# Performance work log

Hardware: AMD Instinct MI355X
Metric: run time of the kernel (lower is better)

## Reference

```python
import jax, jax.numpy as jnp
import numpy as np

EPS = 1e-5

def _layernorm(x, gamma, beta):
    mu = jnp.mean(x, axis=-1, keepdims=True)
    var = jnp.var(x, axis=-1, keepdims=True)
    return (x - mu) * jax.lax.rsqrt(var + EPS) * gamma + beta

def setup_inputs() -> dict:
    key = jax.random.key(0)
    ks = jax.random.split(key, 6)
    bs, t, dim = 4, 2048, 1024
    x = jax.random.normal(ks[0], (bs, t, dim), dtype=jnp.float32)
    # shared LayerNorm params (same module applied twice in forward)
    ln_gamma = jnp.ones((dim,), dtype=jnp.float32)
    ln_beta = jnp.zeros((dim,), dtype=jnp.float32)
    # Linear params, stored as (in, out)
    w1 = jax.random.normal(ks[1], (dim, 2 * dim), dtype=jnp.float32) / np.sqrt(dim)
    b1 = jax.random.normal(ks[2], (2 * dim,), dtype=jnp.float32) * 0.01
    w2 = jax.random.normal(ks[3], (2 * dim, dim), dtype=jnp.float32) / np.sqrt(2 * dim)
    b2 = jax.random.normal(ks[4], (dim,), dtype=jnp.float32) * 0.01
    return {"x": x, "ln_gamma": ln_gamma, "ln_beta": ln_beta,
            "w1": w1, "b1": b1, "w2": w2, "b2": b2}

def reference(x, ln_gamma, ln_beta, w1, b1, w2, b2):
    # x: [bs, t, f]
    y = _layernorm(x, ln_gamma, ln_beta)
    y = jax.nn.gelu(jnp.einsum('btf,fh->bth', y, w1) + b1, approximate=False)
    y = jnp.einsum('bth,hf->btf', y, w2) + b2
    # attention-like quadratic mix (no softmax): (x @ x^T) @ y
    scores = jnp.einsum('btf,bsf->bts', x, x)          # [bs, t, t]
    y = jnp.einsum('bts,bsf->btf', scores, y)
    y = x + y
    y = _layernorm(y, ln_gamma, ln_beta)
    return y
```

## Files before the change

kernel.cpp:

```cpp
#include <hip/hip_runtime.h>
#include <hip/hip_fp16.h>

typedef _Float16 f16;
typedef _Float16 f16x8 __attribute__((ext_vector_type(8)));
typedef _Float16 f16x4 __attribute__((ext_vector_type(4)));
typedef float f32x4 __attribute__((ext_vector_type(4)));

#define LN_EPS 1e-5f

__device__ __forceinline__ float erf_fast(float x) {
    const float ax = __builtin_fabsf(x);
    const float t = 1.0f / (1.0f + 0.3275911f * ax);
    const float y = t * (0.254829592f +
                    t * (-0.284496736f +
                    t * (1.421413741f +
                    t * (-1.453152027f +
                    t * 1.061405429f))));
    const float r = 1.0f - y * __expf(-ax * ax);
    return __builtin_copysignf(r, x);
}

__device__ __forceinline__ float gelu_exact(float v) {
    return 0.5f * v * (1.0f + erf_fast(v * 0.70710678118654752440f));
}

__device__ __forceinline__ void gload_lds16(const f16* g, f16* l) {
    __builtin_amdgcn_global_load_lds(
        (const __attribute__((address_space(1))) unsigned int*)(g),
        (__attribute__((address_space(3))) unsigned int*)(l),
        16, 0, 0);
}

__global__ __launch_bounds__(256)
void ln_cast_kernel(const float* __restrict__ x,
                    const float* __restrict__ gamma,
                    const float* __restrict__ beta,
                    f16* __restrict__ y_h,
                    f16* __restrict__ x_h) {
    const int row = blockIdx.x;
    const int t = threadIdx.x;
    const size_t base = (size_t)row * 1024;
    float4 v = ((const float4*)(x + base))[t];
    float s  = v.x + v.y + v.z + v.w;
    float s2 = v.x*v.x + v.y*v.y + v.z*v.z + v.w*v.w;
    #pragma unroll
    for (int off = 32; off > 0; off >>= 1) {
        s  += __shfl_down(s, off, 64);
        s2 += __shfl_down(s2, off, 64);
    }
    __shared__ float ls[4], ls2[4];
    const int wid = t >> 6;
    if ((t & 63) == 0) { ls[wid] = s; ls2[wid] = s2; }
    __syncthreads();
    if (t == 0) {
        ls[0]  = ls[0] + ls[1] + ls[2] + ls[3];
        ls2[0] = ls2[0] + ls2[1] + ls2[2] + ls2[3];
    }
    __syncthreads();
    const float mu   = ls[0] * (1.0f / 1024.0f);
    const float var  = ls2[0] * (1.0f / 1024.0f) - mu * mu;
    const float rstd = rsqrtf(var + LN_EPS);
    const float4 g  = ((const float4*)gamma)[t];
    const float4 bt = ((const float4*)beta)[t];
    f16x4 yo, xo;
    yo[0] = (f16)((v.x - mu) * rstd * g.x + bt.x);
    yo[1] = (f16)((v.y - mu) * rstd * g.y + bt.y);
    yo[2] = (f16)((v.z - mu) * rstd * g.z + bt.z);
    yo[3] = (f16)((v.w - mu) * rstd * g.w + bt.w);
    xo[0] = (f16)v.x; xo[1] = (f16)v.y; xo[2] = (f16)v.z; xo[3] = (f16)v.w;
    *(f16x4*)(y_h + base + t * 4) = yo;
    *(f16x4*)(x_h + base + t * 4) = xo;
}

__global__ __launch_bounds__(256)
void ln_final_kernel(const float* __restrict__ pre,
                     const float* __restrict__ gamma,
                     const float* __restrict__ beta,
                     float* __restrict__ out) {
    const int row = blockIdx.x;
    const int t = threadIdx.x;
    const size_t base = (size_t)row * 1024;
    float4 v = ((const float4*)(pre + base))[t];
    float s  = v.x + v.y + v.z + v.w;
    float s2 = v.x*v.x + v.y*v.y + v.z*v.z + v.w*v.w;
    #pragma unroll
    for (int off = 32; off > 0; off >>= 1) {
        s  += __shfl_down(s, off, 64);
        s2 += __shfl_down(s2, off, 64);
    }
    __shared__ float ls[4], ls2[4];
    const int wid = t >> 6;
    if ((t & 63) == 0) { ls[wid] = s; ls2[wid] = s2; }
    __syncthreads();
    if (t == 0) {
        ls[0]  = ls[0] + ls[1] + ls[2] + ls[3];
        ls2[0] = ls2[0] + ls2[1] + ls2[2] + ls2[3];
    }
    __syncthreads();
    const float mu   = ls[0] * (1.0f / 1024.0f);
    const float var  = ls2[0] * (1.0f / 1024.0f) - mu * mu;
    const float rstd = rsqrtf(var + LN_EPS);
    const float4 g  = ((const float4*)gamma)[t];
    const float4 bt = ((const float4*)beta)[t];
    float4 o;
    o.x = (v.x - mu) * rstd * g.x + bt.x;
    o.y = (v.y - mu) * rstd * g.y + bt.y;
    o.z = (v.z - mu) * rstd * g.z + bt.z;
    o.w = (v.w - mu) * rstd * g.w + bt.w;
    ((float4*)(out + base))[t] = o;
}

__global__ __launch_bounds__(256)
void transpose_cast_kernel(const float* __restrict__ src,
                           f16* __restrict__ dst, int R, int C) {
    __shared__ float tile[32][33];
    const int c0 = blockIdx.x * 32, r0 = blockIdx.y * 32;
    const int tx = threadIdx.x & 31, ty = threadIdx.x >> 5;
    #pragma unroll
    for (int i = 0; i < 4; ++i) {
        const int r = ty + i * 8;
        tile[r][tx] = src[(size_t)(r0 + r) * C + c0 + tx];
    }
    __syncthreads();
    #pragma unroll
    for (int i = 0; i < 4; ++i) {
        const int r = ty + i * 8;
        dst[(size_t)(c0 + r) * R + r0 + tx] = (f16)tile[tx][r];
    }
}

__global__ __launch_bounds__(256)
void transpose_f16_kernel(const f16* __restrict__ src,
                          f16* __restrict__ dst, int R, int C) {
    __shared__ f16 tile[32][33];
    const size_t zb = (size_t)blockIdx.z * R * C;
    src += zb; dst += zb;
    const int c0 = blockIdx.x * 32, r0 = blockIdx.y * 32;
    const int tx = threadIdx.x & 31, ty = threadIdx.x >> 5;
    #pragma unroll
    for (int i = 0; i < 4; ++i) {
        const int r = ty + i * 8;
        tile[r][tx] = src[(size_t)(r0 + r) * C + c0 + tx];
    }
    __syncthreads();
    #pragma unroll
    for (int i = 0; i < 4; ++i) {
        const int r = ty + i * 8;
        dst[(size_t)(c0 + r) * R + r0 + tx] = tile[tx][r];
    }
}

template <int EPI>
__global__ __launch_bounds__(512, 2)
void gemm256_nt_kernel(const f16* __restrict__ A, const f16* __restrict__ Bt,
                       const float* __restrict__ bias, f16* __restrict__ outH,
                       int M, int N, int K) {
    __shared__ __attribute__((aligned(16))) f16 sAbuf[2][256 * 64];
    __shared__ __attribute__((aligned(16))) f16 sBbuf[2][256 * 64];

    const int m0 = blockIdx.x * 256;
    const int n0 = blockIdx.y * 256;
    const int t = threadIdx.x;
    const int l = t & 63;
    const int wid = t >> 6;
    const int wr = wid >> 2;
    const int wc = wid & 3;
    const int rl = l & 15;
    const int g  = l >> 4;
    const int nk = K >> 6;

    const int rowS = wid * 16 + (l >> 3);
    const int kbS  = ((l & 7) ^ ((l >> 3) & 7)) * 8;
    const f16* pA = A  + (size_t)(m0 + rowS) * K + kbS;
    const f16* pB = Bt + (size_t)(n0 + rowS) * K + kbS;
    const int ldsS = wid * 1024;

    const int rA = wr * 128 + rl;
    const int rB = wc * 64 + rl;
    const int swk0 = ((g)     ^ (rl & 7)) * 8;
    const int swk1 = ((4 + g) ^ (rl & 7)) * 8;

    f32x4 acc[8][4] = {};

    const long long hstep = (long long)128 * K;

    auto stgA = [&](f16* dst, int h, int kc) {
        const f16* s = pA + (size_t)h * hstep + kc * 64;
        f16* d = dst + h * 8192 + ldsS;
        gload_lds16(s, d);
        gload_lds16(s + 8 * K, d + 512);
    };
    auto stgB = [&](f16* dst, int h, int kc) {
        const f16* s = pB + (size_t)h * hstep + kc * 64;
        f16* d = dst + h * 8192 + ldsS;
        gload_lds16(s, d);
        gload_lds16(s + 8 * K, d + 512);
    };

    f16* bufA0 = sAbuf[0]; f16* bufA1 = sAbuf[1];
    f16* bufB0 = sBbuf[0]; f16* bufB1 = sBbuf[1];

    const int t1 = (nk > 1) ? 1 : 0;
    stgA(bufA0, 0, 0); stgA(bufA0, 1, 0);
    stgB(bufB0, 0, 0); stgB(bufB0, 1, 0);
    stgB(bufB1, 0, t1); stgB(bufB1, 1, t1);
    stgA(bufA1, 0, t1);
    asm volatile("s_waitcnt vmcnt(6)" ::: "memory");
    __builtin_amdgcn_s_barrier();

    f16 *Ac = bufA0, *Ao = bufA1, *Bc = bufB0, *Bo = bufB1;

    f16x8 a[4][2], b0r[2][2], b1r[2][2];

    for (int kt = 0; kt < nk; ++kt) {
        const int kt1 = (kt + 1 < nk) ? kt + 1 : nk - 1;
        const int kt2 = (kt + 2 < nk) ? kt + 2 : nk - 1;

        #pragma unroll
        for (int fm = 0; fm < 4; ++fm) {
            a[fm][0] = *(const f16x8*)(Ac + (rA + fm * 16) * 64 + swk0);
            a[fm][1] = *(const f16x8*)(Ac + (rA + fm * 16) * 64 + swk1);
        }
        #pragma unroll
        for (int fn = 0; fn < 2; ++fn) {
            b0r[fn][0] = *(const f16x8*)(Bc + (rB + fn * 16) * 64 + swk0);
            b0r[fn][1] = *(const f16x8*)(Bc + (rB + fn * 16) * 64 + swk1);
        }
        stgA(Ao, 1, kt1);
        __builtin_amdgcn_s_barrier();
        asm volatile("s_waitcnt lgkmcnt(0)" ::: "memory");
        __builtin_amdgcn_sched_barrier(0);
        __builtin_amdgcn_s_setprio(1);
        #pragma unroll
        for (int fm = 0; fm < 4; ++fm)
            #pragma unroll
            for (int fn = 0; fn < 2; ++fn) {
                acc[fm][fn] = __builtin_amdgcn_mfma_f32_16x16x32_f16(a[fm][0], b0r[fn][0], acc[fm][fn], 0, 0, 0);
                acc[fm][fn] = __builtin_amdgcn_mfma_f32_16x16x32_f16(a[fm][1], b0r[fn][1], acc[fm][fn], 0, 0, 0);
            }
        __builtin_amdgcn_s_setprio(0);
        __builtin_amdgcn_s_barrier();

        #pragma unroll
        for (int fn = 0; fn < 2; ++fn) {
            b1r[fn][0] = *(const f16x8*)(Bc + (rB + (fn + 2) * 16) * 64 + swk0);
            b1r[fn][1] = *(const f16x8*)(Bc + (rB + (fn + 2) * 16) * 64 + swk1);
        }
        __builtin_amdgcn_s_barrier();
        asm volatile("s_waitcnt lgkmcnt(0)" ::: "memory");
        __builtin_amdgcn_sched_barrier(0);
        __builtin_amdgcn_s_setprio(1);
        #pragma unroll
        for (int fm = 0; fm < 4; ++fm)
            #pragma unroll
            for (int fn = 0; fn < 2; ++fn) {
                acc[fm][fn + 2] = __builtin_amdgcn_mfma_f32_16x16x32_f16(a[fm][0], b1r[fn][0], acc[fm][fn + 2], 0, 0, 0);
                acc[fm][fn + 2] = __builtin_amdgcn_mfma_f32_16x16x32_f16(a[fm][1], b1r[fn][1], acc[fm][fn + 2], 0, 0, 0);
            }
        __builtin_amdgcn_s_setprio(0);
        __builtin_amdgcn_s_barrier();

        #pragma unroll
        for (int fm = 0; fm < 4; ++fm) {
            a[fm][0] = *(const f16x8*)(Ac + (rA + (fm + 4) * 16) * 64 + swk0);
            a[fm][1] = *(const f16x8*)(Ac + (rA + (fm + 4) * 16) * 64 + swk1);
        }
        stgB(Bc, 0, kt2);
        __builtin_amdgcn_s_barrier();
        asm volatile("s_waitcnt lgkmcnt(0)" ::: "memory");
        __builtin_amdgcn_sched_barrier(0);
        __builtin_amdgcn_s_setprio(1);
        #pragma unroll
        for (int fm = 0; fm < 4; ++fm)
            #pragma unroll
            for (int fn = 0; fn < 2; ++fn) {
                acc[fm + 4][fn + 2] = __builtin_amdgcn_mfma_f32_16x16x32_f16(a[fm][0], b1r[fn][0], acc[fm + 4][fn + 2], 0, 0, 0);
                acc[fm + 4][fn + 2] = __builtin_amdgcn_mfma_f32_16x16x32_f16(a[fm][1], b1r[fn][1], acc[fm + 4][fn + 2], 0, 0, 0);
            }
        __builtin_amdgcn_s_setprio(0);
        __builtin_amdgcn_s_barrier();

        stgB(Bc, 1, kt2);
        stgA(Ac, 0, kt2);
        __builtin_amdgcn_s_barrier();
        __builtin_amdgcn_s_setprio(1);
        #pragma unroll
        for (int fm = 0; fm < 4; ++fm)
            #pragma unroll
            for (int fn = 0; fn < 2; ++fn) {
                acc[fm + 4][fn] = __builtin_amdgcn_mfma_f32_16x16x32_f16(a[fm][0], b0r[fn][0], acc[fm + 4][fn], 0, 0, 0);
                acc[fm + 4][fn] = __builtin_amdgcn_mfma_f32_16x16x32_f16(a[fm][1], b0r[fn][1], acc[fm + 4][fn], 0, 0, 0);
            }
        __builtin_amdgcn_s_setprio(0);
        asm volatile("s_waitcnt vmcnt(6)" ::: "memory");
        __builtin_amdgcn_s_barrier();

        f16* tp;
        tp = Ac; Ac = Ao; Ao = tp;
        tp = Bc; Bc = Bo; Bo = tp;
    }
    asm volatile("s_waitcnt vmcnt(0)" ::: "memory");

    #pragma unroll
    for (int fm = 0; fm < 8; ++fm) {
        #pragma unroll
        for (int fn = 0; fn < 4; ++fn) {
            const int col = n0 + wc * 64 + fn * 16 + rl;
            const float bv = bias[col];
            #pragma unroll
            for (int r = 0; r < 4; ++r) {
                const int row = m0 + wr * 128 + fm * 16 + g * 4 + r;
                const float v = acc[fm][fn][r] + bv;
                outH[(size_t)row * N + col] = (f16)gelu_exact(v);
            }
        }
    }
}

template <int EPI>
__global__ __launch_bounds__(256, 3)
void gemm_nt_kernel(const f16* __restrict__ A, const f16* __restrict__ Bt,
                    const float* __restrict__ bias,
                    const float* __restrict__ xadd,
                    f16* __restrict__ outH, float* __restrict__ outF,
                    int M, int N, int K,
                    long long batchA, long long batchB, long long batchC) {
    __shared__ __attribute__((aligned(16))) f16 sA[3][128 * 32];
    __shared__ __attribute__((aligned(16))) f16 sB[3][128 * 32];

    const int z = blockIdx.z;
    A  += (size_t)z * batchA;
    Bt += (size_t)z * batchB;

    const int m0 = blockIdx.x * 128;
    const int n0 = blockIdx.y * 128;
    const int t = threadIdx.x;
    const int l = t & 63;
    const int wid = t >> 6;
    const int wm = (wid >> 1) * 64;
    const int wn = (wid & 1) * 64;

    f32x4 acc[4][4] = {};

    const int rl = l & 15;
    const int nk = K >> 5;

    const int row0 = t >> 2;
    const int kb = ((t & 3) ^ (row0 & 3)) * 8;
    const f16* Ag0 = A  + (size_t)(m0 + row0) * K + kb;
    const f16* Ag1 = A  + (size_t)(m0 + row0 + 64) * K + kb;
    const f16* Bg0 = Bt + (size_t)(n0 + row0) * K + kb;
    const f16* Bg1 = Bt + (size_t)(n0 + row0 + 64) * K + kb;
    const int lo0 = wid * 512;
    const int lo1 = 2048 + wid * 512;

    const int swk = (((l >> 4) ^ (rl & 3))) * 8;

    gload_lds16(Ag0,      sA[0] + lo0);
    gload_lds16(Ag1,      sA[0] + lo1);
    gload_lds16(Bg0,      sB[0] + lo0);
    gload_lds16(Bg1,      sB[0] + lo1);
    gload_lds16(Ag0 + 32, sA[1] + lo0);
    gload_lds16(Ag1 + 32, sA[1] + lo1);
    gload_lds16(Bg0 + 32, sB[1] + lo0);
    gload_lds16(Bg1 + 32, sB[1] + lo1);

    f16 *curA = sA[0], *nxtA = sA[1], *farA = sA[2];
    f16 *curB = sB[0], *nxtB = sB[1], *farB = sB[2];

    for (int kt = 0; kt < nk; ++kt) {
        asm volatile("s_waitcnt vmcnt(4)" ::: "memory");
        __builtin_amdgcn_s_barrier();

        const int ktn = (kt + 2 < nk) ? kt + 2 : nk - 1;
        const int kof = ktn * 32;
        gload_lds16(Ag0 + kof, farA + lo0);
        gload_lds16(Ag1 + kof, farA + lo1);
        gload_lds16(Bg0 + kof, farB + lo0);
        gload_lds16(Bg1 + kof, farB + lo1);

        f16x8 a[4], b[4];
        #pragma unroll
        for (int f = 0; f < 4; ++f) {
            a[f] = *(const f16x8*)&curA[(wm + f * 16 + rl) * 32 + swk];
            b[f] = *(const f16x8*)&curB[(wn + f * 16 + rl) * 32 + swk];
        }
        #pragma unroll
        for (int fm = 0; fm < 4; ++fm)
            #pragma unroll
            for (int fn = 0; fn < 4; ++fn)
                acc[fm][fn] = __builtin_amdgcn_mfma_f32_16x16x32_f16(
                    a[fm], b[fn], acc[fm][fn], 0, 0, 0);

        f16* tA = curA; curA = nxtA; nxtA = farA; farA = tA;
        f16* tB = curB; curB = nxtB; nxtB = farB; farB = tB;
    }
    asm volatile("s_waitcnt vmcnt(0)" ::: "memory");

    const int rh = l >> 4;
    const float* xaddz = xadd;
    f16* outHz = outH;
    float* outFz = outF;
    if (EPI == 3) {
        outFz += (size_t)z * batchC;
        xaddz += (size_t)z * batchC;
    } else if (EPI == 2) {
        outHz += (size_t)z * batchC;
    }
    #pragma unroll
    for (int fm = 0; fm < 4; ++fm) {
        #pragma unroll
        for (int fn = 0; fn < 4; ++fn) {
            const int col = n0 + wn + fn * 16 + rl;
            if (EPI == 1) {
                const int row0o = m0 + wm + fm * 16 + rh * 4;
                const int zz = row0o >> 11;
                const int rr = row0o & 2047;
                const float bv = bias[col];
                f16x4 o;
                #pragma unroll
                for (int r = 0; r < 4; ++r) o[r] = (f16)(acc[fm][fn][r] + bv);
                *(f16x4*)(outH + ((size_t)zz * N + col) * 2048 + rr) = o;
            } else {
                #pragma unroll
                for (int r = 0; r < 4; ++r) {
                    const int row = m0 + wm + fm * 16 + rh * 4 + r;
                    float v = acc[fm][fn][r];
                    const size_t idx = (size_t)row * N + col;
                    if (EPI == 2) {
                        outHz[idx] = (f16)v;
                    } else {
                        outFz[idx] = v + xaddz[idx];
                    }
                }
            }
        }
    }
}

extern "C" void kernel_launch(void* const* d_in, const int* in_sizes, int n_in,
                              void* d_out, int out_size, void* d_ws, size_t ws_size,
                              hipStream_t stream) {
    const float* x     = (const float*)d_in[0];
    const float* gamma = (const float*)d_in[1];
    const float* beta  = (const float*)d_in[2];
    const float* w1    = (const float*)d_in[3];
    const float* b1    = (const float*)d_in[4];
    const float* w2    = (const float*)d_in[5];
    const float* b2    = (const float*)d_in[6];
    float* out = (float*)d_out;

    const int BS = 4, T = 2048, DIM = 1024, HID = 2048;
    const int M = BS * T;
    const long long MB = 1024 * 1024;

    char* ws = (char*)d_ws;
    f16*   x_h  = (f16*)(ws + 0 * MB);
    f16*   y_h  = (f16*)(ws + 16 * MB);
    f16*   h    = (f16*)(ws + 32 * MB);
    float* pre  = (float*)h;
    f16*   y2t  = (f16*)(ws + 64 * MB);
    f16*   x_t  = (f16*)(ws + 80 * MB);
    f16*   G    = (f16*)(ws + 96 * MB);
    f16*   w1t  = (f16*)(ws + 104 * MB);
    f16*   w2t  = (f16*)(ws + 108 * MB);

    ln_cast_kernel<<<M, 256, 0, stream>>>(x, gamma, beta, y_h, x_h);

    transpose_cast_kernel<<<dim3(HID / 32, DIM / 32), 256, 0, stream>>>(w1, w1t, DIM, HID);
    transpose_cast_kernel<<<dim3(DIM / 32, HID / 32), 256, 0, stream>>>(w2, w2t, HID, DIM);

    gemm256_nt_kernel<0><<<dim3(M / 256, HID / 256), 512, 0, stream>>>(
        y_h, w1t, b1, h, M, HID, DIM);

    gemm_nt_kernel<1><<<dim3(M / 128, DIM / 128, 1), 256, 0, stream>>>(
        h, w2t, b2, nullptr, y2t, nullptr, M, DIM, HID, 0, 0, 0);

    transpose_f16_kernel<<<dim3(DIM / 32, T / 32, BS), 256, 0, stream>>>(x_h, x_t, T, DIM);

    gemm_nt_kernel<2><<<dim3(DIM / 128, DIM / 128, BS), 256, 0, stream>>>(
        y2t, x_t, nullptr, nullptr, G, nullptr, DIM, DIM, T,
        (long long)DIM * T, (long long)DIM * T, (long long)DIM * DIM);

    gemm_nt_kernel<3><<<dim3(T / 128, DIM / 128, BS), 256, 0, stream>>>(
        x_h, G, nullptr, x, nullptr, pre, T, DIM, DIM,
        (long long)T * DIM, (long long)DIM * DIM, (long long)T * DIM);

    ln_final_kernel<<<M, 256, 0, stream>>>(pre, gamma, beta, out);
}
```

Baseline: 212.2 us.

## Add 256x128 K64 GEMM kernel with interleaved staging for second and final GEMMs

Adds a 512-thread GEMM kernel with 256x128 output tiles and 64-wide K steps, triple-buffered LDS filled by direct global-to-LDS loads that are interleaved between MFMA groups with priority hints. The second MLP GEMM and the final scores-times-y GEMM now use it, which cuts per-block overhead and raises operand reuse per LDS load. The old 128x128 kernel is reduced to the plain f16-output case. The larger tiles need much more LDS (144 KB per block) and halve the block count, which may reduce occupancy and wave balance across CUs.

```diff
diff --git a/kernel.cpp b/kernel.cpp
--- a/kernel.cpp
+++ b/kernel.cpp
@@ -318,11 +318,186 @@
 }
 
 template <int EPI>
+__global__ __launch_bounds__(512, 2)
+void gemm256x128_nt_kernel(const f16* __restrict__ A, const f16* __restrict__ Bt,
+                           const float* __restrict__ bias,
+                           const float* __restrict__ xadd,
+                           f16* __restrict__ outH, float* __restrict__ outF,
+                           int M, int N, int K,
+                           long long batchA, long long batchB, long long batchC) {
+    __shared__ __attribute__((aligned(16))) f16 sA[3][256 * 64];
+    __shared__ __attribute__((aligned(16))) f16 sB[3][128 * 64];
+
+    const int z = blockIdx.z;
+    A  += (size_t)z * batchA;
+    Bt += (size_t)z * batchB;
+
+    const int m0 = blockIdx.x * 256;
+    const int n0 = blockIdx.y * 128;
+    const int t = threadIdx.x;
+    const int l = t & 63;
+    const int wid = t >> 6;
+    const int wr = wid >> 1;
+    const int wc = wid & 1;
+    const int rl = l & 15;
+    const int g  = l >> 4;
+    const int nk = K >> 6;
+
+    const int rowS = t >> 3;
+    const int kbS  = ((t & 7) ^ (rowS & 7)) * 8;
+    const f16* pA = A  + (size_t)(m0 + rowS) * K + kbS;
+    const f16* pB = Bt + (size_t)(n0 + rowS) * K + kbS;
+    const int ldsS = wid * 512;
+
+    const int rA = wr * 64 + rl;
+    const int rB = wc * 64 + rl;
+    const int swk0 = ((g)     ^ (rl & 7)) * 8;
+    const int swk1 = ((4 + g) ^ (rl & 7)) * 8;
+
+    f32x4 acc[4][4] = {};
+
+    auto stgA = [&](f16* dst, int u, int kc) {
+        gload_lds16(pA + (size_t)u * 64 * K + kc * 64, dst + u * 4096 + ldsS);
+    };
+    auto stgB = [&](f16* dst, int u, int kc) {
+        gload_lds16(pB + (size_t)u * 64 * K + kc * 64, dst + u * 4096 + ldsS);
+    };
+
+    const int t1 = (nk > 1) ? 1 : 0;
+    #pragma unroll
+    for (int u = 0; u < 4; ++u) stgA(sA[0], u, 0);
+    #pragma unroll
+    for (int u = 0; u < 2; ++u) stgB(sB[0], u, 0);
+    #pragma unroll
+    for (int u = 0; u < 4; ++u) stgA(sA[1], u, t1);
+    #pragma unroll
+    for (int u = 0; u < 2; ++u) stgB(sB[1], u, t1);
+
+    f16 *curA = sA[0], *nxtA = sA[1], *farA = sA[2];
+    f16 *curB = sB[0], *nxtB = sB[1], *farB = sB[2];
+
+    f16x8 a[4][2], b[4][2];
+
+    for (int kt = 0; kt < nk; ++kt) {
+        asm volatile("s_waitcnt vmcnt(6)" ::: "memory");
+        __builtin_amdgcn_s_barrier();
+
+        const int kt2 = (kt + 2 < nk) ? kt + 2 : nk - 1;
+
+        #pragma unroll
+        for (int fm = 0; fm < 2; ++fm) {
+            a[fm][0] = *(const f16x8*)(curA + (rA + fm * 16) * 64 + swk0);
+            a[fm][1] = *(const f16x8*)(curA + (rA + fm * 16) * 64 + swk1);
+        }
+        #pragma unroll
+        for (int fn = 0; fn < 2; ++fn) {
+            b[fn][0] = *(const f16x8*)(curB + (rB + fn * 16) * 64 + swk0);
+            b[fn][1] = *(const f16x8*)(curB + (rB + fn * 16) * 64 + swk1);
+        }
+        stgA(farA, 0, kt2);
+        stgA(farA, 1, kt2);
+        asm volatile("s_waitcnt lgkmcnt(0)" ::: "memory");
+        __builtin_amdgcn_sched_barrier(0);
+        __builtin_amdgcn_s_setprio(1);
+        #pragma unroll
+        for (int fm = 0; fm < 2; ++fm)
+            #pragma unroll
+            for (int fn = 0; fn < 2; ++fn) {
+                acc[fm][fn] = __builtin_amdgcn_mfma_f32_16x16x32_f16(a[fm][0], b[fn][0], acc[fm][fn], 0, 0, 0);
+                acc[fm][fn] = __builtin_amdgcn_mfma_f32_16x16x32_f16(a[fm][1], b[fn][1], acc[fm][fn], 0, 0, 0);
+            }
+        __builtin_amdgcn_s_setprio(0);
+
+        #pragma unroll
+        for (int fn = 2; fn < 4; ++fn) {
+            b[fn][0] = *(const f16x8*)(curB + (rB + fn * 16) * 64 + swk0);
+            b[fn][1] = *(const f16x8*)(curB + (rB + fn * 16) * 64 + swk1);
+        }
+        stgA(farA, 2, kt2);
+        stgA(farA, 3, kt2);
+        asm volatile("s_waitcnt lgkmcnt(0)" ::: "memory");
+        __builtin_amdgcn_sched_barrier(0);
+        __builtin_amdgcn_s_setprio(1);
+        #pragma unroll
+        for (int fm = 0; fm < 2; ++fm)
+            #pragma unroll
+            for (int fn = 2; fn < 4; ++fn) {
+                acc[fm][fn] = __builtin_amdgcn_mfma_f32_16x16x32_f16(a[fm][0], b[fn][0], acc[fm][fn], 0, 0, 0);
+                acc[fm][fn] = __builtin_amdgcn_mfma_f32_16x16x32_f16(a[fm][1], b[fn][1], acc[fm][fn], 0, 0, 0);
+            }
+        __builtin_amdgcn_s_setprio(0);
+
+        #pragma unroll
+        for (int fm = 2; fm < 4; ++fm) {
+            a[fm][0] = *(const f16x8*)(curA + (rA + fm * 16) * 64 + swk0);
+            a[fm][1] = *(const f16x8*)(curA + (rA + fm * 16) * 64 + swk1);
+        }
+        stgB(farB, 0, kt2);
+        stgB(farB, 1, kt2);
+        asm volatile("s_waitcnt lgkmcnt(0)" ::: "memory");
+        __builtin_amdgcn_sched_barrier(0);
+        __builtin_amdgcn_s_setprio(1);
+        #pragma unroll
+        for (int fm = 2; fm < 4; ++fm)
+            #pragma unroll
+            for (int fn = 2; fn < 4; ++fn) {
+                acc[fm][fn] = __builtin_amdgcn_mfma_f32_16x16x32_f16(a[fm][0], b[fn][0], acc[fm][fn], 0, 0, 0);
+                acc[fm][fn] = __builtin_amdgcn_mfma_f32_16x16x32_f16(a[fm][1], b[fn][1], acc[fm][fn], 0, 0, 0);
+            }
+        __builtin_amdgcn_s_setprio(0);
+
+        __builtin_amdgcn_s_setprio(1);
+        #pragma unroll
+        for (int fm = 2; fm < 4; ++fm)
+            #pragma unroll
+            for (int fn = 0; fn < 2; ++fn) {
+                acc[fm][fn] = __builtin_amdgcn_mfma_f32_16x16x32_f16(a[fm][0], b[fn][0], acc[fm][fn], 0, 0, 0);
+                acc[fm][fn] = __builtin_amdgcn_mfma_f32_16x16x32_f16(a[fm][1], b[fn][1], acc[fm][fn], 0, 0, 0);
+            }
+        __builtin_amdgcn_s_setprio(0);
+
+        f16* tp;
+        tp = curA; curA = nxtA; nxtA = farA; farA = tp;
+        tp = curB; curB = nxtB; nxtB = farB; farB = tp;
+    }
+    asm volatile("s_waitcnt vmcnt(0)" ::: "memory");
+
+    const float* xaddz = xadd;
+    float* outFz = outF;
+    if (EPI == 3) {
+        outFz += (size_t)z * batchC;
+        xaddz += (size_t)z * batchC;
+    }
+    #pragma unroll
+    for (int fm = 0; fm < 4; ++fm) {
+        #pragma unroll
+        for (int fn = 0; fn < 4; ++fn) {
+            const int col = n0 + wc * 64 + fn * 16 + rl;
+            if (EPI == 1) {
+                const int row0 = m0 + wr * 64 + fm * 16 + g * 4;
+                const int zz = row0 >> 11;
+                const int rr = row0 & 2047;
+                const float bv = bias[col];
+                f16x4 o;
+                #pragma unroll
+                for (int r = 0; r < 4; ++r) o[r] = (f16)(acc[fm][fn][r] + bv);
+                *(f16x4*)(outH + ((size_t)zz * N + col) * 2048 + rr) = o;
+            } else {
+                #pragma unroll
+                for (int r = 0; r < 4; ++r) {
+                    const int row = m0 + wr * 64 + fm * 16 + g * 4 + r;
+                    const size_t idx = (size_t)row * N + col;
+                    outFz[idx] = acc[fm][fn][r] + xaddz[idx];
+                }
+            }
+        }
+    }
+}
+
+template <int EPI>
 __global__ __launch_bounds__(256, 3)
 void gemm_nt_kernel(const f16* __restrict__ A, const f16* __restrict__ Bt,
-                    const float* __restrict__ bias,
-                    const float* __restrict__ xadd,
-                    f16* __restrict__ outH, float* __restrict__ outF,
+                    f16* __restrict__ outH,
                     int M, int N, int K,
                     long long batchA, long long batchB, long long batchC) {
     __shared__ __attribute__((aligned(16))) f16 sA[3][128 * 32];
@@ -398,41 +573,16 @@
     asm volatile("s_waitcnt vmcnt(0)" ::: "memory");
 
     const int rh = l >> 4;
-    const float* xaddz = xadd;
-    f16* outHz = outH;
-    float* outFz = outF;
-    if (EPI == 3) {
-        outFz += (size_t)z * batchC;
-        xaddz += (size_t)z * batchC;
-    } else if (EPI == 2) {
-        outHz += (size_t)z * batchC;
-    }
+    f16* outHz = outH + (size_t)z * batchC;
     #pragma unroll
     for (int fm = 0; fm < 4; ++fm) {
         #pragma unroll
         for (int fn = 0; fn < 4; ++fn) {
             const int col = n0 + wn + fn * 16 + rl;
-            if (EPI == 1) {
-                const int row0o = m0 + wm + fm * 16 + rh * 4;
-                const int zz = row0o >> 11;
-                const int rr = row0o & 2047;
-                const float bv = bias[col];
-                f16x4 o;
-                #pragma unroll
-                for (int r = 0; r < 4; ++r) o[r] = (f16)(acc[fm][fn][r] + bv);
-                *(f16x4*)(outH + ((size_t)zz * N + col) * 2048 + rr) = o;
-            } else {
-                #pragma unroll
-                for (int r = 0; r < 4; ++r) {
-                    const int row = m0 + wm + fm * 16 + rh * 4 + r;
-                    float v = acc[fm][fn][r];
-                    const size_t idx = (size_t)row * N + col;
-                    if (EPI == 2) {
-                        outHz[idx] = (f16)v;
-                    } else {
-                        outFz[idx] = v + xaddz[idx];
-                    }
-                }
+            #pragma unroll
+            for (int r = 0; r < 4; ++r) {
+                const int row = m0 + wm + fm * 16 + rh * 4 + r;
+                outHz[(size_t)row * N + col] = (f16)acc[fm][fn][r];
             }
         }
     }
@@ -473,16 +623,16 @@
     gemm256_nt_kernel<0><<<dim3(M / 256, HID / 256), 512, 0, stream>>>(
         y_h, w1t, b1, h, M, HID, DIM);
 
-    gemm_nt_kernel<1><<<dim3(M / 128, DIM / 128, 1), 256, 0, stream>>>(
+    gemm256x128_nt_kernel<1><<<dim3(M / 256, DIM / 128, 1), 512, 0, stream>>>(
         h, w2t, b2, nullptr, y2t, nullptr, M, DIM, HID, 0, 0, 0);
 
     transpose_f16_kernel<<<dim3(DIM / 32, T / 32, BS), 256, 0, stream>>>(x_h, x_t, T, DIM);
 
     gemm_nt_kernel<2><<<dim3(DIM / 128, DIM / 128, BS), 256, 0, stream>>>(
-        y2t, x_t, nullptr, nullptr, G, nullptr, DIM, DIM, T,
+        y2t, x_t, G, DIM, DIM, T,
         (long long)DIM * T, (long long)DIM * T, (long long)DIM * DIM);
 
-    gemm_nt_kernel<3><<<dim3(T / 128, DIM / 128, BS), 256, 0, stream>>>(
+    gemm256x128_nt_kernel<3><<<dim3(T / 256, DIM / 128, BS), 512, 0, stream>>>(
         x_h, G, nullptr, x, nullptr, pre, T, DIM, DIM,
         (long long)T * DIM, (long long)DIM * DIM, (long long)T * DIM);
 
```

After: 198.4 us. 1.07x faster.
